# Kernel tuning notes

Hardware: AMD Instinct MI355X
Metric: run time of the kernel (lower is better)

## Reference

```python
import jax, jax.numpy as jnp
import numpy as np

B = 131072          # batch of fermion configurations
S = 256             # sys_size
NUP = 16            # num_fillings[0]
NDOWN = 16          # num_fillings[1]


def _random_occupancy(rng, b, s, nfill):
    # exactly `nfill` ones per row, uniformly random positions
    r = rng.random((b, s))
    perm_rank = np.argsort(r, axis=1).argsort(axis=1)  # a random permutation per row
    return (perm_rank < nfill).astype(np.float32)


def setup_inputs() -> dict:
    rng = np.random.default_rng(0)
    cfg_up = _random_occupancy(rng, B, S, NUP)
    cfg_down = _random_occupancy(rng, B, S, NDOWN)
    config_fermion = jnp.asarray(np.concatenate([cfg_up, cfg_down], axis=1))  # (B, 2S)
    key = jax.random.key(0)
    k1, k2 = jax.random.split(key)
    states_up = jax.random.normal(k1, (S, NUP), dtype=jnp.float32)
    states_down = jax.random.normal(k2, (S, NDOWN), dtype=jnp.float32)
    return {"config_fermion": config_fermion, "states_up": states_up, "states_down": states_down}


def reference(config_fermion, states_up, states_down):
    s = states_up.shape[0]
    nup = states_up.shape[1]
    ndown = states_down.shape[1]
    cfg_up = config_fermion[:, :s]      # (B, S) of {0,1}
    cfg_down = config_fermion[:, s:]
    # indices of occupied sites, ascending (torch.nonzero order); top_k breaks
    # ties by lowest index, then sort ascending
    idx_up = jnp.sort(jax.lax.top_k(cfg_up, nup)[1], axis=1)        # (B, Nup)
    idx_down = jnp.sort(jax.lax.top_k(cfg_down, ndown)[1], axis=1)  # (B, Ndown)
    mats_up = states_up[idx_up]         # (B, Nup, Nup) gather of orbital rows
    mats_down = states_down[idx_down]   # (B, Ndown, Ndown)
    det_up = jnp.linalg.det(mats_up)
    det_down = jnp.linalg.det(mats_down)
    return det_up * det_down
```

## Files before the change

kernel.cpp:

```cpp
#include <hip/hip_runtime.h>

static __device__ __forceinline__ unsigned umax2(unsigned a, unsigned b) { return a > b ? a : b; }

static __device__ __forceinline__ float qb(float v, int sel) {
    int i = __float_as_int(v), r;
    switch (sel) {
        case 0:  r = __builtin_amdgcn_update_dpp(0, i, 0x00, 0xF, 0xF, true); break;
        case 1:  r = __builtin_amdgcn_update_dpp(0, i, 0x55, 0xF, 0xF, true); break;
        case 2:  r = __builtin_amdgcn_update_dpp(0, i, 0xAA, 0xF, 0xF, true); break;
        default: r = __builtin_amdgcn_update_dpp(0, i, 0xFF, 0xF, 0xF, true); break;
    }
    return __int_as_float(r);
}

static __device__ __forceinline__ int mbcnt64(unsigned long long m, int acc) {
    acc = __builtin_amdgcn_mbcnt_lo((unsigned)m, acc);
    acc = __builtin_amdgcn_mbcnt_hi((unsigned)(m >> 32), acc);
    return acc;
}

__global__ __launch_bounds__(256) void slater_det_main(
    const float* __restrict__ cfg,
    const float* __restrict__ sup,
    const float* __restrict__ sdn,
    float* __restrict__ out,
    unsigned* __restrict__ ws_count,
    unsigned* __restrict__ ws_rec,
    unsigned cap,
    int nchunks)
{
    __shared__ __align__(16) int idx_lds[4][16][16];

    const int tid  = threadIdx.x;
    const int wave = tid >> 6;
    const int lane = tid & 63;
    const int wgid = blockIdx.x * 4 + wave;
    const int nw   = gridDim.x * 4;

    const int g = lane >> 2;
    const int q = lane & 3;
    const float* tab = (g & 1) ? sdn : sup;

    float4 c[8];
    int cur = wgid;
    if (cur >= nchunks) return;

#pragma unroll
    for (int d = 0; d < 8; ++d)
        c[d] = *(const float4*)(cfg + (size_t)cur * 4096 + (size_t)d * 256 + (size_t)lane * 4);

    while (cur < nchunks) {
        const int nxt = cur + nw;

#pragma unroll
        for (int d = 0; d < 8; ++d) {
            float4 v = c[d];
            bool n0 = v.x != 0.f, n1 = v.y != 0.f, n2 = v.z != 0.f, n3 = v.w != 0.f;
            unsigned long long b0 = __ballot(n0);
            unsigned long long b1 = __ballot(n1);
            unsigned long long b2 = __ballot(n2);
            unsigned long long b3 = __ballot(n3);
            int r = mbcnt64(b3, mbcnt64(b2, mbcnt64(b1, mbcnt64(b0, 0))));
            int pos = lane * 4;
            if (n0) idx_lds[wave][d][r] = pos;
            r += n0;
            if (n1) idx_lds[wave][d][r] = pos + 1;
            r += n1;
            if (n2) idx_lds[wave][d][r] = pos + 2;
            r += n2;
            if (n3) idx_lds[wave][d][r] = pos + 3;
        }
#pragma unroll
        for (int d = 0; d < 8; ++d)
            c[d] = *(const float4*)(cfg + (size_t)cur * 4096 + (size_t)(d + 8) * 256 + (size_t)lane * 4);
#pragma unroll
        for (int d = 0; d < 8; ++d) {
            float4 v = c[d];
            bool n0 = v.x != 0.f, n1 = v.y != 0.f, n2 = v.z != 0.f, n3 = v.w != 0.f;
            unsigned long long b0 = __ballot(n0);
            unsigned long long b1 = __ballot(n1);
            unsigned long long b2 = __ballot(n2);
            unsigned long long b3 = __ballot(n3);
            int r = mbcnt64(b3, mbcnt64(b2, mbcnt64(b1, mbcnt64(b0, 0))));
            int pos = lane * 4;
            if (n0) idx_lds[wave][d + 8][r] = pos;
            r += n0;
            if (n1) idx_lds[wave][d + 8][r] = pos + 1;
            r += n1;
            if (n2) idx_lds[wave][d + 8][r] = pos + 2;
            r += n2;
            if (n3) idx_lds[wave][d + 8][r] = pos + 3;
        }
        asm volatile("s_waitcnt lgkmcnt(0)" ::: "memory");

        const int4 ri = *(const int4*)&idx_lds[wave][g][q * 4];
        const int rid[4] = {ri.x, ri.y, ri.z, ri.w};

        float rr[4][16];
#pragma unroll
        for (int j = 0; j < 4; ++j) {
            const float* p = tab + (size_t)rid[j] * 16;
            float4 a = *(const float4*)(p + 0);
            float4 b = *(const float4*)(p + 4);
            float4 e = *(const float4*)(p + 8);
            float4 f = *(const float4*)(p + 12);
            rr[j][0]=a.x;  rr[j][1]=a.y;  rr[j][2]=a.z;  rr[j][3]=a.w;
            rr[j][4]=b.x;  rr[j][5]=b.y;  rr[j][6]=b.z;  rr[j][7]=b.w;
            rr[j][8]=e.x;  rr[j][9]=e.y;  rr[j][10]=e.z; rr[j][11]=e.w;
            rr[j][12]=f.x; rr[j][13]=f.y; rr[j][14]=f.z; rr[j][15]=f.w;
        }

        if (nxt < nchunks) {
#pragma unroll
            for (int d = 0; d < 8; ++d)
                c[d] = *(const float4*)(cfg + (size_t)nxt * 4096 + (size_t)d * 256 + (size_t)lane * 4);
        }

        float det = 1.f;
        float minpiv = 1.f;
#pragma unroll
        for (int k = 0; k < 16; ++k) {
            const int sel = k >> 2;
            const int jp  = k & 3;
            float piv = qb(rr[jp][k], sel);
            det *= piv;
            minpiv = fminf(minpiv, fabsf(piv));
            float inv = __builtin_amdgcn_rcpf(piv);
            float f0 = rr[0][k] * inv;
            float f1 = rr[1][k] * inv;
            float f2 = rr[2][k] * inv;
            float f3 = rr[3][k] * inv;
#pragma unroll
            for (int cc = k + 1; cc < 16; ++cc) {
                float pcc = qb(rr[jp][cc], sel);
                rr[0][cc] = __builtin_fmaf(-f0, pcc, rr[0][cc]);
                rr[1][cc] = __builtin_fmaf(-f1, pcc, rr[1][cc]);
                rr[2][cc] = __builtin_fmaf(-f2, pcc, rr[2][cc]);
                rr[3][cc] = __builtin_fmaf(-f3, pcc, rr[3][cc]);
            }
        }
        bool bad = minpiv < 1e-4f;

        int badflag = bad ? 1 : 0;
        int partnerbad = __shfl_xor(badflag, 4);
        if ((badflag | partnerbad) && (lane & 7) == 0) {
            unsigned slot = atomicAdd(ws_count, 1u);
            if (slot < cap) {
                unsigned* rec = ws_rec + slot * 12;
                rec[0] = (unsigned)(cur * 8 + (lane >> 3));
                const int gU = lane >> 2;
#pragma unroll
                for (int t = 0; t < 4; ++t) {
                    const int* iu = &idx_lds[wave][gU][t * 4];
                    const int* id = &idx_lds[wave][gU | 1][t * 4];
                    rec[1 + t] = (unsigned)iu[0] | ((unsigned)iu[1] << 8)
                               | ((unsigned)iu[2] << 16) | ((unsigned)iu[3] << 24);
                    rec[5 + t] = (unsigned)id[0] | ((unsigned)id[1] << 8)
                               | ((unsigned)id[2] << 16) | ((unsigned)id[3] << 24);
                }
            }
        }

        float prod = det * __shfl_xor(det, 4);
        if ((lane & 7) == 0) out[cur * 8 + (lane >> 3)] = prod;

        cur = nxt;
    }
}

__global__ __launch_bounds__(256) void slater_det_cleanup(
    const float* __restrict__ sup,
    const float* __restrict__ sdn,
    float* __restrict__ out,
    const unsigned* __restrict__ ws_count,
    const unsigned* __restrict__ ws_rec,
    unsigned cap)
{
    unsigned n = *ws_count;
    if (n > cap) n = cap;
    const int tid  = blockIdx.x * 256 + threadIdx.x;
    const int unit = tid >> 3;
    const int nunits = (int)(gridDim.x * 256) >> 3;
    const int l8   = threadIdx.x & 7;
    const int wl   = threadIdx.x & 63;
    const int q    = wl & 3;
    const int gbase = wl & ~3;

    for (unsigned item = unit; item < n; item += nunits) {
        const unsigned* rec = ws_rec + item * 12;
        const unsigned batch = rec[0];
        const int half = l8 >> 2;
        const unsigned pk = rec[1 + half * 4 + q];
        const int rid[4] = { (int)(pk & 255u), (int)((pk >> 8) & 255u),
                             (int)((pk >> 16) & 255u), (int)(pk >> 24) };
        const float* tab = half ? sdn : sup;

        float rr[4][16];
#pragma unroll
        for (int j = 0; j < 4; ++j) {
            const float* p = tab + (size_t)rid[j] * 16;
            float4 a = *(const float4*)(p + 0);
            float4 b = *(const float4*)(p + 4);
            float4 e = *(const float4*)(p + 8);
            float4 f = *(const float4*)(p + 12);
            rr[j][0]=a.x;  rr[j][1]=a.y;  rr[j][2]=a.z;  rr[j][3]=a.w;
            rr[j][4]=b.x;  rr[j][5]=b.y;  rr[j][6]=b.z;  rr[j][7]=b.w;
            rr[j][8]=e.x;  rr[j][9]=e.y;  rr[j][10]=e.z; rr[j][11]=e.w;
            rr[j][12]=f.x; rr[j][13]=f.y; rr[j][14]=f.z; rr[j][15]=f.w;
        }

        unsigned am = 0xFu;
        float fdet = 1.f;
        int flips = 0;
#pragma unroll
        for (int k = 0; k < 16; ++k) {
            unsigned a0 = (__float_as_uint(rr[0][k]) & 0x7FFFFFF0u) | (unsigned)(q*4+0);
            unsigned a1 = (__float_as_uint(rr[1][k]) & 0x7FFFFFF0u) | (unsigned)(q*4+1);
            unsigned a2 = (__float_as_uint(rr[2][k]) & 0x7FFFFFF0u) | (unsigned)(q*4+2);
            unsigned a3 = (__float_as_uint(rr[3][k]) & 0x7FFFFFF0u) | (unsigned)(q*4+3);
            unsigned key0 = (am & 1u) ? a0 : (unsigned)(q*4+0);
            unsigned key1 = (am & 2u) ? a1 : (unsigned)(q*4+1);
            unsigned key2 = (am & 4u) ? a2 : (unsigned)(q*4+2);
            unsigned key3 = (am & 8u) ? a3 : (unsigned)(q*4+3);
            unsigned kloc = umax2(umax2(key0, key1), umax2(key2, key3));
            int jloc = (int)(kloc & 3u);
            float crow[16];
#pragma unroll
            for (int cc = k; cc < 16; ++cc) {
                float t01 = (jloc & 1) ? rr[1][cc] : rr[0][cc];
                float t23 = (jloc & 1) ? rr[3][cc] : rr[2][cc];
                crow[cc] = (jloc & 2) ? t23 : t01;
            }
            unsigned ko = kloc;
            ko = umax2(ko, (unsigned)__shfl_xor((int)ko, 1));
            ko = umax2(ko, (unsigned)__shfl_xor((int)ko, 2));
            int p   = (int)(ko & 15u);
            int src = gbase | (p >> 2);
            float prow[16];
#pragma unroll
            for (int cc = k; cc < 16; ++cc) prow[cc] = __shfl(crow[cc], src);
            float piv = prow[k];
            fdet *= piv;
            int t = p - q * 4;
            unsigned mlt = (t <= 0) ? 0u : ((t >= 4) ? 0xFu : ((1u << t) - 1u));
            int cnt = __popc(am & mlt);
            cnt += __shfl_xor(cnt, 1);
            cnt += __shfl_xor(cnt, 2);
            flips += cnt;
            if (q == (p >> 2)) am &= ~(1u << (p & 3));
            float inv = 1.0f / piv;
            float f0 = rr[0][k] * inv;
            float f1 = rr[1][k] * inv;
            float f2 = rr[2][k] * inv;
            float f3 = rr[3][k] * inv;
#pragma unroll
            for (int cc = k + 1; cc < 16; ++cc) {
                rr[0][cc] = __builtin_fmaf(-f0, prow[cc], rr[0][cc]);
                rr[1][cc] = __builtin_fmaf(-f1, prow[cc], rr[1][cc]);
                rr[2][cc] = __builtin_fmaf(-f2, prow[cc], rr[2][cc]);
                rr[3][cc] = __builtin_fmaf(-f3, prow[cc], rr[3][cc]);
            }
        }
        float det = (flips & 1) ? -fdet : fdet;
        float prod = det * __shfl_xor(det, 4);
        if (l8 == 0) out[batch] = prod;
    }
}

extern "C" void kernel_launch(void* const* d_in, const int* in_sizes, int n_in,
                              void* d_out, int out_size, void* d_ws, size_t ws_size,
                              hipStream_t stream) {
    const float* cfg = (const float*)d_in[0];
    const float* sup = (const float*)d_in[1];
    const float* sdn = (const float*)d_in[2];
    float* outp = (float*)d_out;
    unsigned* ws_count = (unsigned*)d_ws;
    unsigned* ws_rec   = (unsigned*)d_ws + 4;
    unsigned cap = (unsigned)((ws_size - 16) / 48);
    const int B = in_sizes[0] / 512;
    const int nchunks = B / 8;

    hipMemsetAsync(d_ws, 0, 16, stream);
    slater_det_main<<<2048, 256, 0, stream>>>(cfg, sup, sdn, outp,
                                              ws_count, ws_rec, cap, nchunks);
    slater_det_cleanup<<<16, 256, 0, stream>>>(sup, sdn, outp,
                                               ws_count, ws_rec, cap);
}
```

Baseline: 64.51 us.

## Stream config chunks via global_load_lds into double-buffered LDS

Instead of loading each 16 KB configuration chunk into registers in two halves, the kernel now issues direct global-to-LDS loads into a per-wave double buffer. The whole next chunk is prefetched while the current determinant runs, and the grid is halved to 1024 blocks. This aims to free VGPRs, keep more bytes in flight and hide HBM latency behind compute. In exchange, 128 KB of LDS per block sharply limits occupancy, and the vmcnt(0) wait also covers the table gathers.

```diff
diff --git a/kernel.cpp b/kernel.cpp
--- a/kernel.cpp
+++ b/kernel.cpp
@@ -19,7 +19,13 @@
     return acc;
 }
 
-__global__ __launch_bounds__(256) void slater_det_main(
+static __device__ __forceinline__ void gload16(const float* g, void* l) {
+    __builtin_amdgcn_global_load_lds(
+        (const __attribute__((address_space(1))) unsigned*)g,
+        (__attribute__((address_space(3))) unsigned*)l, 16, 0, 0);
+}
+
+__global__ __launch_bounds__(256) void slater_stream(
     const float* __restrict__ cfg,
     const float* __restrict__ sup,
     const float* __restrict__ sdn,
@@ -29,6 +35,7 @@
     unsigned cap,
     int nchunks)
 {
+    __shared__ __align__(16) float buf[4][2][4096];
     __shared__ __align__(16) int idx_lds[4][16][16];
 
     const int tid  = threadIdx.x;
@@ -41,20 +48,26 @@
     const int q = lane & 3;
     const float* tab = (g & 1) ? sdn : sup;
 
-    float4 c[8];
     int cur = wgid;
     if (cur >= nchunks) return;
-
-#pragma unroll
-    for (int d = 0; d < 8; ++d)
-        c[d] = *(const float4*)(cfg + (size_t)cur * 4096 + (size_t)d * 256 + (size_t)lane * 4);
+    int pp = 0;
+
+    {
+        const float* src = cfg + (size_t)cur * 4096 + (size_t)lane * 4;
+#pragma unroll
+        for (int h = 0; h < 16; ++h)
+            gload16(src + h * 256, &buf[wave][0][h * 256]);
+    }
 
     while (cur < nchunks) {
         const int nxt = cur + nw;
 
-#pragma unroll
-        for (int d = 0; d < 8; ++d) {
-            float4 v = c[d];
+        asm volatile("s_waitcnt vmcnt(0)" ::: "memory");
+
+        const float* bp = &buf[wave][pp][0];
+#pragma unroll
+        for (int h = 0; h < 16; ++h) {
+            float4 v = *(const float4*)(bp + h * 256 + lane * 4);
             bool n0 = v.x != 0.f, n1 = v.y != 0.f, n2 = v.z != 0.f, n3 = v.w != 0.f;
             unsigned long long b0 = __ballot(n0);
             unsigned long long b1 = __ballot(n1);
@@ -62,40 +75,18 @@
             unsigned long long b3 = __ballot(n3);
             int r = mbcnt64(b3, mbcnt64(b2, mbcnt64(b1, mbcnt64(b0, 0))));
             int pos = lane * 4;
-            if (n0) idx_lds[wave][d][r] = pos;
+            if (n0) idx_lds[wave][h][r] = pos;
             r += n0;
-            if (n1) idx_lds[wave][d][r] = pos + 1;
+            if (n1) idx_lds[wave][h][r] = pos + 1;
             r += n1;
-            if (n2) idx_lds[wave][d][r] = pos + 2;
+            if (n2) idx_lds[wave][h][r] = pos + 2;
             r += n2;
-            if (n3) idx_lds[wave][d][r] = pos + 3;
-        }
-#pragma unroll
-        for (int d = 0; d < 8; ++d)
-            c[d] = *(const float4*)(cfg + (size_t)cur * 4096 + (size_t)(d + 8) * 256 + (size_t)lane * 4);
-#pragma unroll
-        for (int d = 0; d < 8; ++d) {
-            float4 v = c[d];
-            bool n0 = v.x != 0.f, n1 = v.y != 0.f, n2 = v.z != 0.f, n3 = v.w != 0.f;
-            unsigned long long b0 = __ballot(n0);
-            unsigned long long b1 = __ballot(n1);
-            unsigned long long b2 = __ballot(n2);
-            unsigned long long b3 = __ballot(n3);
-            int r = mbcnt64(b3, mbcnt64(b2, mbcnt64(b1, mbcnt64(b0, 0))));
-            int pos = lane * 4;
-            if (n0) idx_lds[wave][d + 8][r] = pos;
-            r += n0;
-            if (n1) idx_lds[wave][d + 8][r] = pos + 1;
-            r += n1;
-            if (n2) idx_lds[wave][d + 8][r] = pos + 2;
-            r += n2;
-            if (n3) idx_lds[wave][d + 8][r] = pos + 3;
+            if (n3) idx_lds[wave][h][r] = pos + 3;
         }
         asm volatile("s_waitcnt lgkmcnt(0)" ::: "memory");
 
         const int4 ri = *(const int4*)&idx_lds[wave][g][q * 4];
         const int rid[4] = {ri.x, ri.y, ri.z, ri.w};
-
         float rr[4][16];
 #pragma unroll
         for (int j = 0; j < 4; ++j) {
@@ -109,11 +100,13 @@
             rr[j][8]=e.x;  rr[j][9]=e.y;  rr[j][10]=e.z; rr[j][11]=e.w;
             rr[j][12]=f.x; rr[j][13]=f.y; rr[j][14]=f.z; rr[j][15]=f.w;
         }
+        __builtin_amdgcn_sched_barrier(0);
 
         if (nxt < nchunks) {
-#pragma unroll
-            for (int d = 0; d < 8; ++d)
-                c[d] = *(const float4*)(cfg + (size_t)nxt * 4096 + (size_t)d * 256 + (size_t)lane * 4);
+            const float* src = cfg + (size_t)nxt * 4096 + (size_t)lane * 4;
+#pragma unroll
+            for (int h = 0; h < 16; ++h)
+                gload16(src + h * 256, &buf[wave][pp ^ 1][h * 256]);
         }
 
         float det = 1.f;
@@ -165,6 +158,7 @@
         if ((lane & 7) == 0) out[cur * 8 + (lane >> 3)] = prod;
 
         cur = nxt;
+        pp ^= 1;
     }
 }
 
@@ -281,8 +275,8 @@
     const int nchunks = B / 8;
 
     hipMemsetAsync(d_ws, 0, 16, stream);
-    slater_det_main<<<2048, 256, 0, stream>>>(cfg, sup, sdn, outp,
-                                              ws_count, ws_rec, cap, nchunks);
+    slater_stream<<<1024, 256, 0, stream>>>(cfg, sup, sdn, outp,
+                                            ws_count, ws_rec, cap, nchunks);
     slater_det_cleanup<<<16, 256, 0, stream>>>(sup, sdn, outp,
                                                ws_count, ws_rec, cap);
 }
```

New measurement: 111.5 us. 1.73x slower.

## Replace persistent grid loop with one-chunk-per-wave grid and direct-to-LDS loads

Applied to the files above, without the earlier changes.

The persistent grid-stride loop with register prefetch of the next chunk is removed. Each wave now handles exactly one 8-row chunk, and the launch uses B/32 blocks. The second half of each chunk's configuration is fetched with global_load_lds straight into a new 32 KB shared buffer while the first half is scanned from registers. This aims to raise the number of loads in flight and drop the loop overhead, at the cost of much more LDS per block (lower occupancy) and a larger launch. It also drops the nchunks bounds check, so B must be a multiple of 32.

```diff
diff --git a/kernel.cpp b/kernel.cpp
--- a/kernel.cpp
+++ b/kernel.cpp
@@ -19,6 +19,12 @@
     return acc;
 }
 
+static __device__ __forceinline__ void gload16(const float* g, void* l) {
+    __builtin_amdgcn_global_load_lds(
+        (const __attribute__((address_space(1))) unsigned*)g,
+        (__attribute__((address_space(3))) unsigned*)l, 16, 0, 0);
+}
+
 __global__ __launch_bounds__(256) void slater_det_main(
     const float* __restrict__ cfg,
     const float* __restrict__ sup,
@@ -26,146 +32,136 @@
     float* __restrict__ out,
     unsigned* __restrict__ ws_count,
     unsigned* __restrict__ ws_rec,
-    unsigned cap,
-    int nchunks)
+    unsigned cap)
 {
+    __shared__ __align__(16) float hbuf[4][8][256];
     __shared__ __align__(16) int idx_lds[4][16][16];
 
     const int tid  = threadIdx.x;
     const int wave = tid >> 6;
     const int lane = tid & 63;
-    const int wgid = blockIdx.x * 4 + wave;
-    const int nw   = gridDim.x * 4;
+    const int wb0  = (blockIdx.x * 4 + wave) * 8;
 
     const int g = lane >> 2;
     const int q = lane & 3;
     const float* tab = (g & 1) ? sdn : sup;
 
+    const float* src = cfg + (size_t)wb0 * 512 + (size_t)lane * 4;
+
+#pragma unroll
+    for (int h = 0; h < 8; ++h)
+        gload16(src + (size_t)(h + 8) * 256, &hbuf[wave][h][0]);
+
     float4 c[8];
-    int cur = wgid;
-    if (cur >= nchunks) return;
-
 #pragma unroll
     for (int d = 0; d < 8; ++d)
-        c[d] = *(const float4*)(cfg + (size_t)cur * 4096 + (size_t)d * 256 + (size_t)lane * 4);
-
-    while (cur < nchunks) {
-        const int nxt = cur + nw;
-
-#pragma unroll
-        for (int d = 0; d < 8; ++d) {
-            float4 v = c[d];
-            bool n0 = v.x != 0.f, n1 = v.y != 0.f, n2 = v.z != 0.f, n3 = v.w != 0.f;
-            unsigned long long b0 = __ballot(n0);
-            unsigned long long b1 = __ballot(n1);
-            unsigned long long b2 = __ballot(n2);
-            unsigned long long b3 = __ballot(n3);
-            int r = mbcnt64(b3, mbcnt64(b2, mbcnt64(b1, mbcnt64(b0, 0))));
-            int pos = lane * 4;
-            if (n0) idx_lds[wave][d][r] = pos;
-            r += n0;
-            if (n1) idx_lds[wave][d][r] = pos + 1;
-            r += n1;
-            if (n2) idx_lds[wave][d][r] = pos + 2;
-            r += n2;
-            if (n3) idx_lds[wave][d][r] = pos + 3;
-        }
-#pragma unroll
-        for (int d = 0; d < 8; ++d)
-            c[d] = *(const float4*)(cfg + (size_t)cur * 4096 + (size_t)(d + 8) * 256 + (size_t)lane * 4);
-#pragma unroll
-        for (int d = 0; d < 8; ++d) {
-            float4 v = c[d];
-            bool n0 = v.x != 0.f, n1 = v.y != 0.f, n2 = v.z != 0.f, n3 = v.w != 0.f;
-            unsigned long long b0 = __ballot(n0);
-            unsigned long long b1 = __ballot(n1);
-            unsigned long long b2 = __ballot(n2);
-            unsigned long long b3 = __ballot(n3);
-            int r = mbcnt64(b3, mbcnt64(b2, mbcnt64(b1, mbcnt64(b0, 0))));
-            int pos = lane * 4;
-            if (n0) idx_lds[wave][d + 8][r] = pos;
-            r += n0;
-            if (n1) idx_lds[wave][d + 8][r] = pos + 1;
-            r += n1;
-            if (n2) idx_lds[wave][d + 8][r] = pos + 2;
-            r += n2;
-            if (n3) idx_lds[wave][d + 8][r] = pos + 3;
-        }
-        asm volatile("s_waitcnt lgkmcnt(0)" ::: "memory");
-
-        const int4 ri = *(const int4*)&idx_lds[wave][g][q * 4];
-        const int rid[4] = {ri.x, ri.y, ri.z, ri.w};
-
-        float rr[4][16];
-#pragma unroll
-        for (int j = 0; j < 4; ++j) {
-            const float* p = tab + (size_t)rid[j] * 16;
-            float4 a = *(const float4*)(p + 0);
-            float4 b = *(const float4*)(p + 4);
-            float4 e = *(const float4*)(p + 8);
-            float4 f = *(const float4*)(p + 12);
-            rr[j][0]=a.x;  rr[j][1]=a.y;  rr[j][2]=a.z;  rr[j][3]=a.w;
-            rr[j][4]=b.x;  rr[j][5]=b.y;  rr[j][6]=b.z;  rr[j][7]=b.w;
-            rr[j][8]=e.x;  rr[j][9]=e.y;  rr[j][10]=e.z; rr[j][11]=e.w;
-            rr[j][12]=f.x; rr[j][13]=f.y; rr[j][14]=f.z; rr[j][15]=f.w;
-        }
-
-        if (nxt < nchunks) {
-#pragma unroll
-            for (int d = 0; d < 8; ++d)
-                c[d] = *(const float4*)(cfg + (size_t)nxt * 4096 + (size_t)d * 256 + (size_t)lane * 4);
-        }
-
-        float det = 1.f;
-        float minpiv = 1.f;
-#pragma unroll
-        for (int k = 0; k < 16; ++k) {
-            const int sel = k >> 2;
-            const int jp  = k & 3;
-            float piv = qb(rr[jp][k], sel);
-            det *= piv;
-            minpiv = fminf(minpiv, fabsf(piv));
-            float inv = __builtin_amdgcn_rcpf(piv);
-            float f0 = rr[0][k] * inv;
-            float f1 = rr[1][k] * inv;
-            float f2 = rr[2][k] * inv;
-            float f3 = rr[3][k] * inv;
-#pragma unroll
-            for (int cc = k + 1; cc < 16; ++cc) {
-                float pcc = qb(rr[jp][cc], sel);
-                rr[0][cc] = __builtin_fmaf(-f0, pcc, rr[0][cc]);
-                rr[1][cc] = __builtin_fmaf(-f1, pcc, rr[1][cc]);
-                rr[2][cc] = __builtin_fmaf(-f2, pcc, rr[2][cc]);
-                rr[3][cc] = __builtin_fmaf(-f3, pcc, rr[3][cc]);
+        c[d] = *(const float4*)(src + (size_t)d * 256);
+
+#pragma unroll
+    for (int d = 0; d < 8; ++d) {
+        float4 v = c[d];
+        bool n0 = v.x != 0.f, n1 = v.y != 0.f, n2 = v.z != 0.f, n3 = v.w != 0.f;
+        unsigned long long b0 = __ballot(n0);
+        unsigned long long b1 = __ballot(n1);
+        unsigned long long b2 = __ballot(n2);
+        unsigned long long b3 = __ballot(n3);
+        int r = mbcnt64(b3, mbcnt64(b2, mbcnt64(b1, mbcnt64(b0, 0))));
+        int pos = lane * 4;
+        if (n0) idx_lds[wave][d][r] = pos;
+        r += n0;
+        if (n1) idx_lds[wave][d][r] = pos + 1;
+        r += n1;
+        if (n2) idx_lds[wave][d][r] = pos + 2;
+        r += n2;
+        if (n3) idx_lds[wave][d][r] = pos + 3;
+    }
+
+    asm volatile("s_waitcnt vmcnt(0)" ::: "memory");
+    __builtin_amdgcn_sched_barrier(0);
+
+#pragma unroll
+    for (int d = 0; d < 8; ++d) {
+        float4 v = *(const float4*)&hbuf[wave][d][lane * 4];
+        bool n0 = v.x != 0.f, n1 = v.y != 0.f, n2 = v.z != 0.f, n3 = v.w != 0.f;
+        unsigned long long b0 = __ballot(n0);
+        unsigned long long b1 = __ballot(n1);
+        unsigned long long b2 = __ballot(n2);
+        unsigned long long b3 = __ballot(n3);
+        int r = mbcnt64(b3, mbcnt64(b2, mbcnt64(b1, mbcnt64(b0, 0))));
+        int pos = lane * 4;
+        if (n0) idx_lds[wave][d + 8][r] = pos;
+        r += n0;
+        if (n1) idx_lds[wave][d + 8][r] = pos + 1;
+        r += n1;
+        if (n2) idx_lds[wave][d + 8][r] = pos + 2;
+        r += n2;
+        if (n3) idx_lds[wave][d + 8][r] = pos + 3;
+    }
+    asm volatile("s_waitcnt lgkmcnt(0)" ::: "memory");
+
+    const int4 ri = *(const int4*)&idx_lds[wave][g][q * 4];
+    const int rid[4] = {ri.x, ri.y, ri.z, ri.w};
+    float rr[4][16];
+#pragma unroll
+    for (int j = 0; j < 4; ++j) {
+        const float* p = tab + (size_t)rid[j] * 16;
+        float4 a = *(const float4*)(p + 0);
+        float4 b = *(const float4*)(p + 4);
+        float4 e = *(const float4*)(p + 8);
+        float4 f = *(const float4*)(p + 12);
+        rr[j][0]=a.x;  rr[j][1]=a.y;  rr[j][2]=a.z;  rr[j][3]=a.w;
+        rr[j][4]=b.x;  rr[j][5]=b.y;  rr[j][6]=b.z;  rr[j][7]=b.w;
+        rr[j][8]=e.x;  rr[j][9]=e.y;  rr[j][10]=e.z; rr[j][11]=e.w;
+        rr[j][12]=f.x; rr[j][13]=f.y; rr[j][14]=f.z; rr[j][15]=f.w;
+    }
+
+    float det = 1.f;
+    float minpiv = 1.f;
+#pragma unroll
+    for (int k = 0; k < 16; ++k) {
+        const int sel = k >> 2;
+        const int jp  = k & 3;
+        float piv = qb(rr[jp][k], sel);
+        det *= piv;
+        minpiv = fminf(minpiv, fabsf(piv));
+        float inv = __builtin_amdgcn_rcpf(piv);
+        float f0 = rr[0][k] * inv;
+        float f1 = rr[1][k] * inv;
+        float f2 = rr[2][k] * inv;
+        float f3 = rr[3][k] * inv;
+#pragma unroll
+        for (int cc = k + 1; cc < 16; ++cc) {
+            float pcc = qb(rr[jp][cc], sel);
+            rr[0][cc] = __builtin_fmaf(-f0, pcc, rr[0][cc]);
+            rr[1][cc] = __builtin_fmaf(-f1, pcc, rr[1][cc]);
+            rr[2][cc] = __builtin_fmaf(-f2, pcc, rr[2][cc]);
+            rr[3][cc] = __builtin_fmaf(-f3, pcc, rr[3][cc]);
+        }
+    }
+    bool bad = minpiv < 1e-4f;
+
+    int badflag = bad ? 1 : 0;
+    int partnerbad = __shfl_xor(badflag, 4);
+    if ((badflag | partnerbad) && (lane & 7) == 0) {
+        unsigned slot = atomicAdd(ws_count, 1u);
+        if (slot < cap) {
+            unsigned* rec = ws_rec + slot * 12;
+            rec[0] = (unsigned)(wb0 + (lane >> 3));
+            const int gU = lane >> 2;
+#pragma unroll
+            for (int t = 0; t < 4; ++t) {
+                const int* iu = &idx_lds[wave][gU][t * 4];
+                const int* id = &idx_lds[wave][gU | 1][t * 4];
+                rec[1 + t] = (unsigned)iu[0] | ((unsigned)iu[1] << 8)
+                           | ((unsigned)iu[2] << 16) | ((unsigned)iu[3] << 24);
+                rec[5 + t] = (unsigned)id[0] | ((unsigned)id[1] << 8)
+                           | ((unsigned)id[2] << 16) | ((unsigned)id[3] << 24);
             }
         }
-        bool bad = minpiv < 1e-4f;
-
-        int badflag = bad ? 1 : 0;
-        int partnerbad = __shfl_xor(badflag, 4);
-        if ((badflag | partnerbad) && (lane & 7) == 0) {
-            unsigned slot = atomicAdd(ws_count, 1u);
-            if (slot < cap) {
-                unsigned* rec = ws_rec + slot * 12;
-                rec[0] = (unsigned)(cur * 8 + (lane >> 3));
-                const int gU = lane >> 2;
-#pragma unroll
-                for (int t = 0; t < 4; ++t) {
-                    const int* iu = &idx_lds[wave][gU][t * 4];
-                    const int* id = &idx_lds[wave][gU | 1][t * 4];
-                    rec[1 + t] = (unsigned)iu[0] | ((unsigned)iu[1] << 8)
-                               | ((unsigned)iu[2] << 16) | ((unsigned)iu[3] << 24);
-                    rec[5 + t] = (unsigned)id[0] | ((unsigned)id[1] << 8)
-                               | ((unsigned)id[2] << 16) | ((unsigned)id[3] << 24);
-                }
-            }
-        }
-
-        float prod = det * __shfl_xor(det, 4);
-        if ((lane & 7) == 0) out[cur * 8 + (lane >> 3)] = prod;
-
-        cur = nxt;
-    }
+    }
+
+    float prod = det * __shfl_xor(det, 4);
+    if ((lane & 7) == 0) out[wb0 + (lane >> 3)] = prod;
 }
 
 __global__ __launch_bounds__(256) void slater_det_cleanup(
@@ -278,11 +274,11 @@
     unsigned* ws_rec   = (unsigned*)d_ws + 4;
     unsigned cap = (unsigned)((ws_size - 16) / 48);
     const int B = in_sizes[0] / 512;
-    const int nchunks = B / 8;
+    const int blocks = B / 32;
 
     hipMemsetAsync(d_ws, 0, 16, stream);
-    slater_det_main<<<2048, 256, 0, stream>>>(cfg, sup, sdn, outp,
-                                              ws_count, ws_rec, cap, nchunks);
+    slater_det_main<<<blocks, 256, 0, stream>>>(cfg, sup, sdn, outp,
+                                                ws_count, ws_rec, cap);
     slater_det_cleanup<<<16, 256, 0, stream>>>(sup, sdn, outp,
                                                ws_count, ws_rec, cap);
 }
```

Result: slower. 68.41 us (+6.0%).
